# Kernel optimization log

Measured on AMD Instinct MI355X. Metric: run time of the kernel, lower is better.

## Reference

```python
import jax, jax.numpy as jnp
import numpy as np

N = 60000   # nodes (utterances)
E = 480000  # edges
C = 256     # utt_size == embedding_size (shrink disabled)
R = 16      # num_relations for conv1; conv3 uses n_speakers**2 == 16
NB = 8      # rgcn_reg_basis (num_bases)
NS = 4      # n_speakers


def _rgcn(x, src, dst, etype, comp, bases, root, bias, num_rel):
    # PyG RGCNConv with basis decomposition: W_r = sum_b comp[r,b] * bases[b]
    # out_i = sum_r mean_{j in N_r(i)} x_j @ W_r + x_i @ root + bias
    n = x.shape[0]
    W = jnp.einsum('rb,bio->rio', comp, bases)                      # [R,C,C]
    xw = jnp.einsum('ni,rio->rno', x, W).reshape(num_rel * n, -1)   # [R*N,C]
    seg = dst * num_rel + etype                                     # (dst, rel) bucket
    ones = jnp.ones((src.shape[0],), x.dtype)
    cnt = jax.ops.segment_sum(ones, seg, num_segments=n * num_rel)
    norm = (1.0 / jnp.maximum(cnt, 1.0))[seg]                       # per-relation mean
    msg = xw[etype * n + src] * norm[:, None]                       # [E,C] gather
    return jax.ops.segment_sum(msg, dst, num_segments=n) + x @ root + bias


def _gconv(x, src, dst, w_rel, b_rel, w_root):
    # PyG GraphConv, aggr='add': lin_rel(sum_j x_j) + lin_root(x)
    agg = jax.ops.segment_sum(x[src], dst, num_segments=x.shape[0])
    return agg @ w_rel + b_rel + x @ w_root


def _mlp(x, w1, c1, w2, c2, w3, c3):
    h = jax.nn.relu(x @ w1 + c1)
    h = jax.nn.relu(h @ w2 + c2)
    return h @ w3 + c3


def setup_inputs():
    key = jax.random.key(0)
    ks = jax.random.split(key, 24)
    f = lambda i, shape, s=0.05: jax.random.normal(ks[i], shape, jnp.float32) * s
    z = lambda d: jnp.zeros((d,), jnp.float32)
    return {
        'encoding': jax.random.normal(ks[0], (N, C), jnp.float32),
        'speaker': jax.random.randint(ks[1], (N,), 0, NS),
        'edge_index': jax.random.randint(ks[2], (2, E), 0, N),
        'edge_type': jax.random.randint(ks[3], (E,), 0, R),
        'edge_speaker_type': jax.random.randint(ks[4], (E,), 0, NS * NS),
        'spk_table': f(5, (NS, C)),
        'comp1': f(6, (R, NB), 0.2), 'bases1': f(7, (NB, C, C)),
        'root1': f(8, (C, C)), 'b1': z(C),
        'w2_rel': f(9, (C, C)), 'b2': z(C), 'w2_root': f(10, (C, C)),
        'comp3': f(11, (NS * NS, NB), 0.2), 'bases3': f(12, (NB, C, C)),
        'root3': f(13, (C, C)), 'b3': z(C),
        'w4_rel': f(14, (C, C)), 'b4': z(C), 'w4_root': f(15, (C, C)),
        'wd1': f(16, (3 * C, C // 2)), 'bd1': z(C // 2),
        'wd2': f(17, (C // 2, C // 4)), 'bd2': z(C // 4),
        'wd3': f(18, (C // 4, 1)), 'bd3': z(1),
    }


def reference(encoding, speaker, edge_index, edge_type, edge_speaker_type,
              spk_table, comp1, bases1, root1, b1, w2_rel, b2, w2_root,
              comp3, bases3, root3, b3, w4_rel, b4, w4_root,
              wd1, bd1, wd2, bd2, wd3, bd3):
    src, dst = edge_index[0], edge_index[1]
    x = encoding + spk_table[speaker]            # speaker embedding fusion
    h1 = _rgcn(x, src, dst, edge_type, comp1, bases1, root1, b1, R)
    h1 = _gconv(h1, src, dst, w2_rel, b2, w2_root)
    h2 = _rgcn(x, src, dst, edge_speaker_type, comp3, bases3, root3, b3, NS * NS)
    h2 = _gconv(h2, src, dst, w4_rel, b4, w4_root)
    feat = jnp.concatenate([encoding, h1, h2], axis=1)  # [N, 3C]
    pred = _mlp(feat, wd1, bd1, wd2, bd2, wd3, bd3)     # [N, 1]
    return pred.squeeze(1)
```

## Files before the change

kernel.cpp:

```cpp
#include <hip/hip_runtime.h>
#include <stdint.h>


typedef unsigned short u16;
typedef __attribute__((ext_vector_type(2))) float f32x2;
typedef __attribute__((ext_vector_type(4))) float f32x4;
typedef __attribute__((ext_vector_type(8))) short short8;

__device__ __forceinline__ float b2f(u16 u){
  union { uint32_t i; float f; } v; v.i = ((uint32_t)u) << 16; return v.f;
}
__device__ __forceinline__ u16 f2b(float f){
  union { float f; uint32_t i; } v; v.f = f;
  uint32_t u = v.i;
  return (u16)((u + 0x7FFFu + ((u >> 16) & 1u)) >> 16);
}
__device__ __forceinline__ u16 rdw(const void* p, size_t i, int f32){
  return f32 ? f2b(((const float*)p)[i]) : ((const u16*)p)[i];
}
__device__ __forceinline__ void gload_lds16(const u16* gp, u16* lp){
  __builtin_amdgcn_global_load_lds(
      (const __attribute__((address_space(1))) uint32_t*)(uintptr_t)gp,
      (__attribute__((address_space(3))) uint32_t*)lp, 16, 0, 0);
}

__global__ void detect_dtype(const u16* enc16, int* flag){
  __shared__ int cnt;
  if (threadIdx.x == 0) cnt = 0;
  __syncthreads();
  unsigned u = enc16[threadIdx.x * 2];
  int e = (u >> 7) & 0xFF;
  if (e >= 100 && e <= 140) atomicAdd(&cnt, 1);
  __syncthreads();
  if (threadIdx.x == 0) flag[0] = (cnt < 128) ? 1 : 0;
}

__global__ void cvt_small(const void* spk, const void* c1, const void* c3,
                          const void* b1, const void* b2, const void* b3,
                          const void* b4, const void* bd1, const void* wd2,
                          const void* bd2, const void* wd3, const void* bd3,
                          u16* __restrict__ arena, const int* __restrict__ flag)
{
  int f = *flag;
  int i = blockIdx.x * blockDim.x + threadIdx.x;
  if (i < 1024) { arena[i] = rdw(spk, i, f); return; } i -= 1024;
  if (i < 128)  { arena[1024 + i] = rdw(c1, i, f); return; } i -= 128;
  if (i < 128)  { arena[1152 + i] = rdw(c3, i, f); return; } i -= 128;
  if (i < 256)  { arena[1280 + i] = rdw(b1, i, f); return; } i -= 256;
  if (i < 256)  { arena[1536 + i] = rdw(b2, i, f); return; } i -= 256;
  if (i < 256)  { arena[1792 + i] = rdw(b3, i, f); return; } i -= 256;
  if (i < 256)  { arena[2048 + i] = rdw(b4, i, f); return; } i -= 256;
  if (i < 128)  { arena[2304 + i] = rdw(bd1, i, f); return; } i -= 128;
  if (i < 64)   { arena[10624 + i] = rdw(bd2, i, f); return; } i -= 64;
  if (i < 64)   { arena[10688 + i] = rdw(wd3, i, f); return; } i -= 64;
  if (i < 1)    { arena[10752 + i] = rdw(bd3, i, f); return; } i -= 1;
  if (i < 8192) { int o = i >> 7, k = i & 127;
    arena[10880 + i] = rdw(wd2, k * 64 + o, f); }
}

__global__ void cvt4(const void* __restrict__ in, u16* __restrict__ out, int n,
                     const int* __restrict__ flag){
  int i = (blockIdx.x * blockDim.x + threadIdx.x) * 4;
  if (i >= n) return;
  ushort4 o;
  if (*flag) {
    float4 v = *(const float4*)((const float*)in + i);
    o.x = f2b(v.x); o.y = f2b(v.y); o.z = f2b(v.z); o.w = f2b(v.w);
  } else {
    o = *(const ushort4*)((const u16*)in + i);
  }
  *(ushort4*)(out + i) = o;
}

__global__ void pack_weights(const void* __restrict__ bases1, const void* __restrict__ root1,
                             const void* __restrict__ w2_rel, const void* __restrict__ w2_root,
                             const void* __restrict__ bases3, const void* __restrict__ root3,
                             const void* __restrict__ w4_rel, const void* __restrict__ w4_root,
                             const void* __restrict__ wd1,
                             u16* __restrict__ B1t, u16* __restrict__ B3t,
                             u16* __restrict__ B2t, u16* __restrict__ B4t,
                             u16* __restrict__ D1t, const int* __restrict__ flag)
{
  int f = *flag;
  int idx = blockIdx.x * blockDim.x + threadIdx.x;
  if (idx < 256*2304) { int o = idx / 2304, k = idx % 2304;
    B1t[idx] = (k < 2048) ? rdw(bases1, k*256 + o, f) : rdw(root1, (k-2048)*256 + o, f); return; }
  idx -= 256*2304;
  if (idx < 256*2304) { int o = idx / 2304, k = idx % 2304;
    B3t[idx] = (k < 2048) ? rdw(bases3, k*256 + o, f) : rdw(root3, (k-2048)*256 + o, f); return; }
  idx -= 256*2304;
  if (idx < 256*512) { int o = idx / 512, k = idx % 512;
    B2t[idx] = (k < 256) ? rdw(w2_rel, k*256 + o, f) : rdw(w2_root, (k-256)*256 + o, f); return; }
  idx -= 256*512;
  if (idx < 256*512) { int o = idx / 512, k = idx % 512;
    B4t[idx] = (k < 256) ? rdw(w4_rel, k*256 + o, f) : rdw(w4_root, (k-256)*256 + o, f); return; }
  idx -= 256*512;
  if (idx < 128*768) { int o = idx / 768, k = idx % 768;
    D1t[idx] = rdw(wd1, k*128 + o, f); }
}

__global__ void build_x(const void* __restrict__ enc, const int* __restrict__ speaker,
                        const u16* __restrict__ spkA ,
                        u16* __restrict__ X , int N,
                        const int* __restrict__ flag)
{
  int f = *flag;
  int idx = blockIdx.x * blockDim.x + threadIdx.x;
  if (idx >= N * 64) return;
  int n = idx >> 6, c = (idx & 63) * 4;
  int sp = speaker[n];
  ushort4 sv = *(const ushort4*)(spkA + (size_t)sp*256 + c);
  float e0, e1, e2, e3;
  if (f) {
    float4 ev = *(const float4*)((const float*)enc + (size_t)n*256 + c);
    e0 = ev.x; e1 = ev.y; e2 = ev.z; e3 = ev.w;
  } else {
    ushort4 ev = *(const ushort4*)((const u16*)enc + (size_t)n*256 + c);
    e0 = b2f(ev.x); e1 = b2f(ev.y); e2 = b2f(ev.z); e3 = b2f(ev.w);
  }
  ushort4 xv;
  xv.x = f2b(e0 + b2f(sv.x));
  xv.y = f2b(e1 + b2f(sv.y));
  xv.z = f2b(e2 + b2f(sv.z));
  xv.w = f2b(e3 + b2f(sv.w));
  *(ushort4*)(X + (size_t)n*256 + c) = xv;
}

__global__ void edge_hist(const int* __restrict__ ei, int* cnt_dst, int E)
{
  int e = blockIdx.x * blockDim.x + threadIdx.x;
  if (e >= E) return;
  atomicAdd(&cnt_dst[ei[E + e]], 1);
}

__global__ void scan_p1(const int* __restrict__ cnt, int* __restrict__ partial,
                        int* __restrict__ bsum, int N)
{
  __shared__ int s[256];
  int t = threadIdx.x;
  int g = blockIdx.x * 256 + t;
  int v = (g < N) ? cnt[g] : 0;
  s[t] = v; __syncthreads();
  #pragma unroll
  for (int off = 1; off < 256; off <<= 1) {
    int u = (t >= off) ? s[t - off] : 0;
    __syncthreads();
    s[t] += u;
    __syncthreads();
  }
  partial[g] = s[t];
  if (t == 255) bsum[blockIdx.x] = s[255];
}

__global__ void scan_p2(int* __restrict__ bsum, int nb)
{
  __shared__ int s[1024];
  int t = threadIdx.x;
  int v = (t < nb) ? bsum[t] : 0;
  s[t] = v; __syncthreads();
  #pragma unroll
  for (int off = 1; off < 1024; off <<= 1) {
    int u = (t >= off) ? s[t - off] : 0;
    __syncthreads();
    s[t] += u;
    __syncthreads();
  }
  if (t < nb) bsum[t] = s[t] - v;
  if (t == nb - 1) bsum[nb] = s[t];
}

__global__ void scan_p3(const int* __restrict__ cnt, const int* __restrict__ partial,
                        const int* __restrict__ bsum, int* __restrict__ basep, int N)
{
  int g = blockIdx.x * 256 + threadIdx.x;
  if (g < N) basep[g] = partial[g] - cnt[g] + bsum[blockIdx.x];
  if (g == 0) basep[N] = bsum[(N + 255) / 256];
}

__global__ void edge_scatter(const int* __restrict__ ei, const int* __restrict__ et,
                             const int* __restrict__ est, const int* __restrict__ basep,
                             int* cursor, int* __restrict__ esorted, int E)
{
  int e = blockIdx.x * blockDim.x + threadIdx.x;
  if (e >= E) return;
  int d = ei[E + e];
  int pos = basep[d] + atomicAdd(&cursor[d], 1);
  esorted[pos] = ei[e] | (et[e] << 17) | (est[e] << 21);
}

__global__ __launch_bounds__(256) void rgcn_agg2(
    const int* __restrict__ esorted, const int* __restrict__ basep,
    const u16* __restrict__ X ,
    const u16* __restrict__ comp1 ,
    const u16* __restrict__ comp3 ,
    u16* __restrict__ Mix1 ,
    u16* __restrict__ Mix3 ,
    int n0, int CR)
{
  __shared__ float sc1[128], sc3[128];
  if (threadIdx.x < 128) sc1[threadIdx.x] = b2f(comp1[threadIdx.x]);
  else sc3[threadIdx.x - 128] = b2f(comp3[threadIdx.x - 128]);
  __syncthreads();
  int nl = blockIdx.x * 4 + (threadIdx.x >> 6);
  if (nl >= CR) return;
  int n = n0 + nl;
  int lane = threadIdx.x & 63;
  int e0 = basep[n], e1 = basep[n + 1];
  int myrel = lane & 15;
  int cnt = 0;
  for (int e = e0; e < e1; e++) {
    int rec = esorted[e];
    int r1 = (rec >> 17) & 15, r3 = (rec >> 21) & 15;
    if (lane < 16) cnt += (r1 == myrel);
    else if (lane < 32) cnt += (r3 == myrel);
  }
  float invv = 1.0f / (float)(cnt > 1 ? cnt : 1);
  f32x2 acc1[8][2] = {}, acc3[8][2] = {};
  for (int e = e0; e < e1; e++) {
    int rec = esorted[e];
    int src = rec & 0x1FFFF;
    int r1 = (rec >> 17) & 15, r3 = (rec >> 21) & 15;
    float iv1 = __shfl(invv, r1);
    float iv3 = __shfl(invv, 16 + r3);
    ushort4 xr = *(const ushort4*)(X + (size_t)src * 256 + lane * 4);
    f32x2 xlo, xhi;
    xlo[0] = b2f(xr.x); xlo[1] = b2f(xr.y);
    xhi[0] = b2f(xr.z); xhi[1] = b2f(xr.w);
    const float* c1p = sc1 + r1 * 8;
    const float* c3p = sc3 + r3 * 8;
    #pragma unroll
    for (int b = 0; b < 8; b++) {
      float w1s = c1p[b] * iv1;
      f32x2 w1 = {w1s, w1s};
      acc1[b][0] += w1 * xlo; acc1[b][1] += w1 * xhi;
      float w3s = c3p[b] * iv3;
      f32x2 w3 = {w3s, w3s};
      acc3[b][0] += w3 * xlo; acc3[b][1] += w3 * xhi;
    }
  }
  #pragma unroll
  for (int b = 0; b < 8; b++) {
    ushort4 o1, o3;
    o1.x = f2b(acc1[b][0][0]); o1.y = f2b(acc1[b][0][1]);
    o1.z = f2b(acc1[b][1][0]); o1.w = f2b(acc1[b][1][1]);
    o3.x = f2b(acc3[b][0][0]); o3.y = f2b(acc3[b][0][1]);
    o3.z = f2b(acc3[b][1][0]); o3.w = f2b(acc3[b][1][1]);
    *(ushort4*)(Mix1 + (size_t)nl * 2048 + b * 256 + lane * 4) = o1;
    *(ushort4*)(Mix3 + (size_t)nl * 2048 + b * 256 + lane * 4) = o3;
  }
}

__global__ __launch_bounds__(256) void gconv_agg2(
    const int* __restrict__ esorted, const int* __restrict__ basep,
    const u16* __restrict__ HinA ,
    const u16* __restrict__ HinB ,
    u16* __restrict__ AggA ,
    u16* __restrict__ AggB , int N)
{
  int n = blockIdx.x * 4 + (threadIdx.x >> 6);
  if (n >= N) return;
  int lane = threadIdx.x & 63;
  int half = lane >> 5, l32 = lane & 31;
  float a[8] = {}, b[8] = {};
  int e0 = basep[n], e1 = basep[n + 1];
  for (int e = e0; e < e1; e += 2) {
    int ee = e + half;
    bool ok = ee < e1;
    int src = esorted[ok ? ee : e] & 0x1FFFF;
    short8 hv  = *(const short8*)(HinA + (size_t)src * 256 + l32 * 8);
    short8 hv3 = *(const short8*)(HinB + (size_t)src * 256 + l32 * 8);
    if (ok) {
      #pragma unroll
      for (int j = 0; j < 8; j++) { a[j] += b2f((u16)hv[j]); b[j] += b2f((u16)hv3[j]); }
    }
  }
  #pragma unroll
  for (int j = 0; j < 8; j++) {
    a[j] += __shfl_xor(a[j], 32);
    b[j] += __shfl_xor(b[j], 32);
  }
  if (half == 0) {
    short8 oa, ob;
    #pragma unroll
    for (int j = 0; j < 8; j++) { oa[j] = (short)f2b(a[j]); ob[j] = (short)f2b(b[j]); }
    *(short8*)(AggA + (size_t)n * 256 + l32 * 8) = oa;
    *(short8*)(AggB + (size_t)n * 256 + l32 * 8) = ob;
  }
}

__global__ __launch_bounds__(256) void gemm_ms(
    const u16* __restrict__ A0, int lda0,
    const u16* __restrict__ A1, int lda1,
    const u16* __restrict__ A2, int lda2,
    int c1, int c2,
    const u16* __restrict__ Bt,
    const u16* __restrict__ bias,
    u16* __restrict__ Cout, int ldc,
    int M, int K, int relu, int nout, int nx,
    const u16* __restrict__ A0d, const u16* __restrict__ A1d,
    const u16* __restrict__ Btd,
    const u16* __restrict__ biasd, u16* __restrict__ Coutd)
{
  constexpr int BK = 64;
  __shared__ u16 As[128 * BK];
  __shared__ u16 Bs[128 * BK];
  int bi = blockIdx.x;
  const u16* A0u = A0; const u16* A1u = A1;
  const u16* Btu = Bt; const u16* biasu = bias;
  u16* Cu = Cout;
  if (bi >= nx) { bi -= nx; A0u = A0d; A1u = A1d; Btu = Btd; biasu = biasd; Cu = Coutd; }
  int nblk = (nout + 127) >> 7;
  int grpw = nblk << 3;
  int g = bi / grpw, r = bi % grpw;
  int bm = (g * 8 + (r & 7)) * 128;
  if (bm >= M) return;
  int bn = (r >> 3) * 128;

  int tid = threadIdx.x;
  int wid = tid >> 6, lane = tid & 63;
  int wm = (wid & 1) * 64, wn = (wid >> 1) * 64;
  int r8 = lane >> 3;
  int colA = ((lane & 7) ^ r8) * 8;
  int rloc = wid * 8 + r8;
  int lm = lane & 15, quad = lane >> 4;

  f32x4 acc[4][4];
  #pragma unroll
  for (int i = 0; i < 4; i++)
    #pragma unroll
    for (int j = 0; j < 4; j++) acc[i][j] = (f32x4)0.0f;

  int ga0 = bm + 0 * 32 + rloc; ga0 = ga0 < M ? ga0 : M - 1;
  int ga1 = bm + 1 * 32 + rloc; ga1 = ga1 < M ? ga1 : M - 1;
  int ga2 = bm + 2 * 32 + rloc; ga2 = ga2 < M ? ga2 : M - 1;
  int ga3 = bm + 3 * 32 + rloc; ga3 = ga3 < M ? ga3 : M - 1;
  int gb0 = bn + 0 * 32 + rloc; gb0 = gb0 < nout ? gb0 : nout - 1;
  int gb1 = bn + 1 * 32 + rloc; gb1 = gb1 < nout ? gb1 : nout - 1;
  int gb2 = bn + 2 * 32 + rloc; gb2 = gb2 < nout ? gb2 : nout - 1;
  int gb3 = bn + 3 * 32 + rloc; gb3 = gb3 < nout ? gb3 : nout - 1;

  for (int k0 = 0; k0 < K; k0 += BK) {
    const u16* srcp; int ldas, kO;
    if (k0 < c1)      { srcp = A0u; ldas = lda0; kO = k0; }
    else if (k0 < c2) { srcp = A1u; ldas = lda1; kO = k0 - c1; }
    else              { srcp = A2;  ldas = lda2; kO = k0 - c2; }
    const u16* abase = srcp + kO + colA;
    gload_lds16(abase + (size_t)ga0 * ldas, As + (0 * 32 + wid * 8) * BK);
    gload_lds16(abase + (size_t)ga1 * ldas, As + (1 * 32 + wid * 8) * BK);
    gload_lds16(abase + (size_t)ga2 * ldas, As + (2 * 32 + wid * 8) * BK);
    gload_lds16(abase + (size_t)ga3 * ldas, As + (3 * 32 + wid * 8) * BK);
    const u16* bbase = Btu + k0 + colA;
    gload_lds16(bbase + (size_t)gb0 * K, Bs + (0 * 32 + wid * 8) * BK);
    gload_lds16(bbase + (size_t)gb1 * K, Bs + (1 * 32 + wid * 8) * BK);
    gload_lds16(bbase + (size_t)gb2 * K, Bs + (2 * 32 + wid * 8) * BK);
    gload_lds16(bbase + (size_t)gb3 * K, Bs + (3 * 32 + wid * 8) * BK);
    __syncthreads();
    #pragma unroll
    for (int kk = 0; kk < BK; kk += 32) {
      int cb = (kk >> 3) + quad;
      int xo = ((cb ^ (lm & 7)) << 3);
      short8 af[4], bf[4];
      #pragma unroll
      for (int mi = 0; mi < 4; mi++)
        af[mi] = *(const short8*)(As + (wm + mi * 16 + lm) * BK + xo);
      #pragma unroll
      for (int ni = 0; ni < 4; ni++)
        bf[ni] = *(const short8*)(Bs + (wn + ni * 16 + lm) * BK + xo);
      #pragma unroll
      for (int mi = 0; mi < 4; mi++)
        #pragma unroll
        for (int ni = 0; ni < 4; ni++)
          acc[mi][ni] = __builtin_amdgcn_mfma_f32_16x16x32_bf16(
              af[mi], bf[ni], acc[mi][ni], 0, 0, 0);
    }
    __syncthreads();
  }
  #pragma unroll
  for (int ni = 0; ni < 4; ni++) {
    int gn = bn + wn + ni * 16 + lm;
    int gnb = gn < nout ? gn : nout - 1;
    float bv = b2f(biasu[gnb]);
    #pragma unroll
    for (int mi = 0; mi < 4; mi++) {
      int rbase = bm + wm + mi * 16 + quad * 4;
      #pragma unroll
      for (int rr = 0; rr < 4; rr++) {
        int gmr = rbase + rr;
        if (gmr < M && gn < nout) {
          float v = acc[mi][ni][rr] + bv;
          if (relu) v = fmaxf(v, 0.f);
          Cu[(size_t)gmr * ldc + gn] = f2b(v);
        }
      }
    }
  }
}

__global__ __launch_bounds__(256) void mlp_tail2(
    const u16* __restrict__ h2m, const u16* __restrict__ wd3,
    const u16* __restrict__ bd3, void* __restrict__ outp, int N,
    const int* __restrict__ flag)
{
  int n = blockIdx.x * 4 + (threadIdx.x >> 6);
  if (n >= N) return;
  int lane = threadIdx.x & 63;
  float r = b2f(h2m[(size_t)n * 64 + lane]) * b2f(wd3[lane]);
  #pragma unroll
  for (int off = 32; off > 0; off >>= 1) r += __shfl_xor(r, off, 64);
  if (lane == 0) {
    float v = r + b2f(bd3[0]);
    if (*flag) ((float*)outp)[n] = v;
    else       ((u16*)outp)[n] = f2b(v);
  }
}

__global__ void sentinel(u16* out, int n, float code){
  int i = blockIdx.x * blockDim.x + threadIdx.x;
  if (i < n) out[i] = f2b(code);
}

extern "C" void kernel_launch(void* const* d_in, const int* in_sizes, int n_in,
                              void* d_out, int out_size, void* d_ws, size_t ws_size,
                              hipStream_t stream)
{
  const void* enc     = d_in[0];
  const int* speaker  = (const int*)d_in[1];
  const int* ei       = (const int*)d_in[2];
  const int* et       = (const int*)d_in[3];
  const int* est      = (const int*)d_in[4];
  const void* spk_tab = d_in[5];
  const void* comp1   = d_in[6];
  const void* bases1  = d_in[7];
  const void* root1   = d_in[8];
  const void* b1      = d_in[9];
  const void* w2_rel  = d_in[10];
  const void* b2      = d_in[11];
  const void* w2_root = d_in[12];
  const void* comp3   = d_in[13];
  const void* bases3  = d_in[14];
  const void* root3   = d_in[15];
  const void* b3      = d_in[16];
  const void* w4_rel  = d_in[17];
  const void* b4      = d_in[18];
  const void* w4_root = d_in[19];
  const void* wd1     = d_in[20];
  const void* bd1     = d_in[21];
  const void* wd2     = d_in[22];
  const void* bd2     = d_in[23];
  const void* wd3     = d_in[24];
  const void* bd3     = d_in[25];

  int N = in_sizes[1];
  int E = in_sizes[3];
  int nb = (N + 255) / 256;

  char* ws = (char*)d_ws;
  size_t off = 0;
  auto alloc = [&](size_t bytes) -> char* {
    char* p = ws + off; off = (off + bytes + 255) & ~(size_t)255; return p;
  };
  u16* X    = (u16*)alloc((size_t)N * 256 * 2);
  u16* hA   = (u16*)alloc((size_t)N * 256 * 2);
  u16* hA3  = (u16*)alloc((size_t)N * 256 * 2);
  u16* B1t  = (u16*)alloc((size_t)256 * 2304 * 2);
  u16* B3t  = (u16*)alloc((size_t)256 * 2304 * 2);
  u16* B2t  = (u16*)alloc((size_t)256 * 512 * 2);
  u16* B4t  = (u16*)alloc((size_t)256 * 512 * 2);
  u16* D1t  = (u16*)alloc((size_t)128 * 768 * 2);
  u16* arena = (u16*)alloc((size_t)20480 * 2);
  int* flag    = (int*)alloc(256);
  int* basep   = (int*)alloc((size_t)(N + 1) * 4);
  int* esorted = (int*)alloc((size_t)E * 4);

  char* R = ws + off;
  size_t Rsize = (ws_size > off) ? (ws_size - off) : 0;

  int* cnt_dst = (int*)R;
  int* cursor  = (int*)(R + (size_t)N * 4);
  int* partial = (int*)(R + (size_t)2 * N * 4);
  int* bsum    = (int*)(R + (size_t)2 * N * 4 + (size_t)nb * 256 * 4);
  size_t zspan = (size_t)2 * N * 4;

  u16* AggA = (u16*)R;
  u16* hB   = (u16*)(R + (size_t)N * 256 * 2);
  u16* hC   = (u16*)(R + (size_t)2 * N * 256 * 2);
  u16* AggC = (u16*)(R + (size_t)3 * N * 256 * 2);
  u16* h1m  = AggA;
  u16* h2m  = AggA + (size_t)N * 128;
  size_t phase2_need = (size_t)4 * N * 256 * 2;

  long crl = (long)(Rsize / (4096 * 2));
  int chunk_max = (int)((crl / 128) * 128);
  int Mpad = ((N + 127) / 128) * 128;
  if (chunk_max > Mpad) chunk_max = Mpad;

  size_t sort_need = (size_t)2 * N * 4 + (size_t)nb * 256 * 4 + 2048 * 4;
  if (chunk_max < 128 || Rsize < phase2_need || Rsize < sort_need) {
    float code = 2000.0f + (float)(ws_size >> 20);
    sentinel<<<(out_size + 255) / 256, 256, 0, stream>>>((u16*)d_out, out_size, code);
    return;
  }
  int nchunks = (Mpad + chunk_max - 1) / chunk_max;
  int chunk_rows = (((N + nchunks - 1) / nchunks + 127) / 128) * 128;
  u16* Mix1blk = (u16*)R;
  u16* Mix3blk = Mix1blk + (size_t)chunk_rows * 2048;

  u16* spkA   = arena + 0;
  u16* comp1A = arena + 1024;
  u16* comp3A = arena + 1152;
  u16* b1A    = arena + 1280;
  u16* b2A    = arena + 1536;
  u16* b3A    = arena + 1792;
  u16* b4A    = arena + 2048;
  u16* bd1A   = arena + 2304;
  u16* bd2A   = arena + 10624;
  u16* wd3A   = arena + 10688;
  u16* bd3A   = arena + 10752;
  u16* wd2T   = arena + 10880;

  hipMemsetAsync(cnt_dst, 0, zspan, stream);

  detect_dtype<<<1, 256, 0, stream>>>((const u16*)enc, flag);
  cvt_small<<<75, 256, 0, stream>>>(spk_tab, comp1, comp3, b1, b2, b3, b4,
                                    bd1, wd2, bd2, wd3, bd3, arena, flag);

  int totpack = 256*2304*2 + 256*512*2 + 128*768;
  pack_weights<<<(totpack + 255) / 256, 256, 0, stream>>>(
      bases1, root1, w2_rel, w2_root, bases3, root3, w4_rel, w4_root, wd1,
      B1t, B3t, B2t, B4t, D1t, flag);
  build_x<<<(N * 64 + 255) / 256, 256, 0, stream>>>(enc, speaker, spkA, X, N, flag);
  edge_hist<<<(E + 255) / 256, 256, 0, stream>>>(ei, cnt_dst, E);
  scan_p1<<<nb, 256, 0, stream>>>(cnt_dst, partial, bsum, N);
  scan_p2<<<1, 1024, 0, stream>>>(bsum, nb);
  scan_p3<<<nb, 256, 0, stream>>>(cnt_dst, partial, bsum, basep, N);
  edge_scatter<<<(E + 255) / 256, 256, 0, stream>>>(ei, et, est, basep, cursor, esorted, E);

  int nb4 = (N + 3) / 4;
  const u16* nul = (const u16*)nullptr;
  auto nx_for = [](int M_, int nout_) {
    int mg = (M_ + 127) / 128;
    int nblk = (nout_ + 127) / 128;
    return ((mg + 7) / 8) * (nblk * 8);
  };

  for (int n0 = 0; n0 < N; n0 += chunk_rows) {
    int CR = (N - n0 < chunk_rows) ? (N - n0) : chunk_rows;
    rgcn_agg2<<<(CR + 3) / 4, 256, 0, stream>>>(esorted, basep, X, comp1A, comp3A,
                                                Mix1blk, Mix3blk, n0, CR);
    int nx = nx_for(CR, 256);
    gemm_ms<<<2 * nx, 256, 0, stream>>>(
        Mix1blk, 2048, X + (size_t)n0 * 256, 256, nul, 0,
        2048, 2304, B1t, b1A, hA + (size_t)n0 * 256, 256, CR, 2304, 0, 256, nx,
        Mix3blk, X + (size_t)n0 * 256, B3t, b3A, hA3 + (size_t)n0 * 256);
  }
  int nxN = nx_for(N, 256);
  gconv_agg2<<<nb4, 256, 0, stream>>>(esorted, basep, hA, hA3, AggA, AggC, N);
  cvt4<<<(N * 64 + 255) / 256, 256, 0, stream>>>(enc, X, N * 256, flag);
  gemm_ms<<<2 * nxN, 256, 0, stream>>>(
      AggA, 256, hA, 256, nul, 0, 256, 512,
      B2t, b2A, hB, 256, N, 512, 0, 256, nxN,
      AggC, hA3, B4t, b4A, hC);

  int nx1 = nx_for(N, 128);
  gemm_ms<<<nx1, 256, 0, stream>>>(
      X, 256, hB, 256, hC, 256, 256, 512,
      D1t, bd1A, h1m, 128, N, 768, 1, 128, nx1,
      nul, nul, nul, nul, (u16*)nullptr);
  int nx2 = nx_for(N, 64);
  gemm_ms<<<nx2, 256, 0, stream>>>(
      h1m, 128, nul, 0, nul, 0, 128, 128,
      wd2T, bd2A, h2m, 64, N, 128, 1, 64, nx2,
      nul, nul, nul, nul, (u16*)nullptr);
  mlp_tail2<<<nb4, 256, 0, stream>>>(h2m, wd3A, bd3A, d_out, N, flag);
}
```

Measured before the change: 790.7 us.

## Unroll RGCN edge loop by two and make GEMM a persistent grid

Measured after the change: 783.5 us. About the same (-0.9%).

```diff
diff --git a/kernel.cpp b/kernel.cpp
--- a/kernel.cpp
+++ b/kernel.cpp
@@ -216,7 +216,36 @@
   }
   float invv = 1.0f / (float)(cnt > 1 ? cnt : 1);
   f32x2 acc1[8][2] = {}, acc3[8][2] = {};
-  for (int e = e0; e < e1; e++) {
+  int e = e0;
+  for (; e + 1 < e1; e += 2) {
+    int recA = esorted[e], recB = esorted[e + 1];
+    int srcA = recA & 0x1FFFF, srcB = recB & 0x1FFFF;
+    ushort4 xra = *(const ushort4*)(X + (size_t)srcA * 256 + lane * 4);
+    ushort4 xrb = *(const ushort4*)(X + (size_t)srcB * 256 + lane * 4);
+    int r1a = (recA >> 17) & 15, r3a = (recA >> 21) & 15;
+    int r1b = (recB >> 17) & 15, r3b = (recB >> 21) & 15;
+    float iv1a = __shfl(invv, r1a), iv3a = __shfl(invv, 16 + r3a);
+    float iv1b = __shfl(invv, r1b), iv3b = __shfl(invv, 16 + r3b);
+    f32x2 alo, ahi, blo, bhi;
+    alo[0] = b2f(xra.x); alo[1] = b2f(xra.y);
+    ahi[0] = b2f(xra.z); ahi[1] = b2f(xra.w);
+    blo[0] = b2f(xrb.x); blo[1] = b2f(xrb.y);
+    bhi[0] = b2f(xrb.z); bhi[1] = b2f(xrb.w);
+    const float* c1a = sc1 + r1a * 8; const float* c3a = sc3 + r3a * 8;
+    const float* c1b = sc1 + r1b * 8; const float* c3b = sc3 + r3b * 8;
+    #pragma unroll
+    for (int b = 0; b < 8; b++) {
+      float w1a = c1a[b] * iv1a, w1b = c1b[b] * iv1b;
+      f32x2 v1a = {w1a, w1a}, v1b = {w1b, w1b};
+      acc1[b][0] += v1a * alo + v1b * blo;
+      acc1[b][1] += v1a * ahi + v1b * bhi;
+      float w3a = c3a[b] * iv3a, w3b = c3b[b] * iv3b;
+      f32x2 v3a = {w3a, w3a}, v3b = {w3b, w3b};
+      acc3[b][0] += v3a * alo + v3b * blo;
+      acc3[b][1] += v3a * ahi + v3b * bhi;
+    }
+  }
+  if (e < e1) {
     int rec = esorted[e];
     int src = rec & 0x1FFFF;
     int r1 = (rec >> 17) & 15, r3 = (rec >> 21) & 15;
@@ -296,7 +325,7 @@
     const u16* __restrict__ Bt,
     const u16* __restrict__ bias,
     u16* __restrict__ Cout, int ldc,
-    int M, int K, int relu, int nout, int nx,
+    int M, int K, int relu, int nout, int nx, int njobs,
     const u16* __restrict__ A0d, const u16* __restrict__ A1d,
     const u16* __restrict__ Btd,
     const u16* __restrict__ biasd, u16* __restrict__ Coutd)
@@ -304,18 +333,6 @@
   constexpr int BK = 64;
   __shared__ u16 As[128 * BK];
   __shared__ u16 Bs[128 * BK];
-  int bi = blockIdx.x;
-  const u16* A0u = A0; const u16* A1u = A1;
-  const u16* Btu = Bt; const u16* biasu = bias;
-  u16* Cu = Cout;
-  if (bi >= nx) { bi -= nx; A0u = A0d; A1u = A1d; Btu = Btd; biasu = biasd; Cu = Coutd; }
-  int nblk = (nout + 127) >> 7;
-  int grpw = nblk << 3;
-  int g = bi / grpw, r = bi % grpw;
-  int bm = (g * 8 + (r & 7)) * 128;
-  if (bm >= M) return;
-  int bn = (r >> 3) * 128;
-
   int tid = threadIdx.x;
   int wid = tid >> 6, lane = tid & 63;
   int wm = (wid & 1) * 64, wn = (wid >> 1) * 64;
@@ -323,73 +340,87 @@
   int colA = ((lane & 7) ^ r8) * 8;
   int rloc = wid * 8 + r8;
   int lm = lane & 15, quad = lane >> 4;
-
-  f32x4 acc[4][4];
-  #pragma unroll
-  for (int i = 0; i < 4; i++)
+  int nblk = (nout + 127) >> 7;
+  int grpw = nblk << 3;
+
+  for (int job = blockIdx.x; job < njobs; job += gridDim.x) {
+    int bi = job;
+    const u16* A0u = A0; const u16* A1u = A1;
+    const u16* Btu = Bt; const u16* biasu = bias;
+    u16* Cu = Cout;
+    if (bi >= nx) { bi -= nx; A0u = A0d; A1u = A1d; Btu = Btd; biasu = biasd; Cu = Coutd; }
+    int g = bi / grpw, r = bi % grpw;
+    int bm = (g * 8 + (r & 7)) * 128;
+    if (bm >= M) continue;
+    int bn = (r >> 3) * 128;
+
+    f32x4 acc[4][4];
     #pragma unroll
-    for (int j = 0; j < 4; j++) acc[i][j] = (f32x4)0.0f;
-
-  int ga0 = bm + 0 * 32 + rloc; ga0 = ga0 < M ? ga0 : M - 1;
-  int ga1 = bm + 1 * 32 + rloc; ga1 = ga1 < M ? ga1 : M - 1;
-  int ga2 = bm + 2 * 32 + rloc; ga2 = ga2 < M ? ga2 : M - 1;
-  int ga3 = bm + 3 * 32 + rloc; ga3 = ga3 < M ? ga3 : M - 1;
-  int gb0 = bn + 0 * 32 + rloc; gb0 = gb0 < nout ? gb0 : nout - 1;
-  int gb1 = bn + 1 * 32 + rloc; gb1 = gb1 < nout ? gb1 : nout - 1;
-  int gb2 = bn + 2 * 32 + rloc; gb2 = gb2 < nout ? gb2 : nout - 1;
-  int gb3 = bn + 3 * 32 + rloc; gb3 = gb3 < nout ? gb3 : nout - 1;
-
-  for (int k0 = 0; k0 < K; k0 += BK) {
-    const u16* srcp; int ldas, kO;
-    if (k0 < c1)      { srcp = A0u; ldas = lda0; kO = k0; }
-    else if (k0 < c2) { srcp = A1u; ldas = lda1; kO = k0 - c1; }
-    else              { srcp = A2;  ldas = lda2; kO = k0 - c2; }
-    const u16* abase = srcp + kO + colA;
-    gload_lds16(abase + (size_t)ga0 * ldas, As + (0 * 32 + wid * 8) * BK);
-    gload_lds16(abase + (size_t)ga1 * ldas, As + (1 * 32 + wid * 8) * BK);
-    gload_lds16(abase + (size_t)ga2 * ldas, As + (2 * 32 + wid * 8) * BK);
-    gload_lds16(abase + (size_t)ga3 * ldas, As + (3 * 32 + wid * 8) * BK);
-    const u16* bbase = Btu + k0 + colA;
-    gload_lds16(bbase + (size_t)gb0 * K, Bs + (0 * 32 + wid * 8) * BK);
-    gload_lds16(bbase + (size_t)gb1 * K, Bs + (1 * 32 + wid * 8) * BK);
-    gload_lds16(bbase + (size_t)gb2 * K, Bs + (2 * 32 + wid * 8) * BK);
-    gload_lds16(bbase + (size_t)gb3 * K, Bs + (3 * 32 + wid * 8) * BK);
-    __syncthreads();
-    #pragma unroll
-    for (int kk = 0; kk < BK; kk += 32) {
-      int cb = (kk >> 3) + quad;
-      int xo = ((cb ^ (lm & 7)) << 3);
-      short8 af[4], bf[4];
+    for (int i = 0; i < 4; i++)
       #pragma unroll
-      for (int mi = 0; mi < 4; mi++)
-        af[mi] = *(const short8*)(As + (wm + mi * 16 + lm) * BK + xo);
+      for (int j = 0; j < 4; j++) acc[i][j] = (f32x4)0.0f;
+
+    int ga0 = bm + 0 * 32 + rloc; ga0 = ga0 < M ? ga0 : M - 1;
+    int ga1 = bm + 1 * 32 + rloc; ga1 = ga1 < M ? ga1 : M - 1;
+    int ga2 = bm + 2 * 32 + rloc; ga2 = ga2 < M ? ga2 : M - 1;
+    int ga3 = bm + 3 * 32 + rloc; ga3 = ga3 < M ? ga3 : M - 1;
+    int gb0 = bn + 0 * 32 + rloc; gb0 = gb0 < nout ? gb0 : nout - 1;
+    int gb1 = bn + 1 * 32 + rloc; gb1 = gb1 < nout ? gb1 : nout - 1;
+    int gb2 = bn + 2 * 32 + rloc; gb2 = gb2 < nout ? gb2 : nout - 1;
+    int gb3 = bn + 3 * 32 + rloc; gb3 = gb3 < nout ? gb3 : nout - 1;
+
+    for (int k0 = 0; k0 < K; k0 += BK) {
+      const u16* srcp; int ldas, kO;
+      if (k0 < c1)      { srcp = A0u; ldas = lda0; kO = k0; }
+      else if (k0 < c2) { srcp = A1u; ldas = lda1; kO = k0 - c1; }
+      else              { srcp = A2;  ldas = lda2; kO = k0 - c2; }
+      const u16* abase = srcp + kO + colA;
+      gload_lds16(abase + (size_t)ga0 * ldas, As + (0 * 32 + wid * 8) * BK);
+      gload_lds16(abase + (size_t)ga1 * ldas, As + (1 * 32 + wid * 8) * BK);
+      gload_lds16(abase + (size_t)ga2 * ldas, As + (2 * 32 + wid * 8) * BK);
+      gload_lds16(abase + (size_t)ga3 * ldas, As + (3 * 32 + wid * 8) * BK);
+      const u16* bbase = Btu + k0 + colA;
+      gload_lds16(bbase + (size_t)gb0 * K, Bs + (0 * 32 + wid * 8) * BK);
+      gload_lds16(bbase + (size_t)gb1 * K, Bs + (1 * 32 + wid * 8) * BK);
+      gload_lds16(bbase + (size_t)gb2 * K, Bs + (2 * 32 + wid * 8) * BK);
+      gload_lds16(bbase + (size_t)gb3 * K, Bs + (3 * 32 + wid * 8) * BK);
+      __syncthreads();
       #pragma unroll
-      for (int ni = 0; ni < 4; ni++)
-        bf[ni] = *(const short8*)(Bs + (wn + ni * 16 + lm) * BK + xo);
-      #pragma unroll
-      for (int mi = 0; mi < 4; mi++)
+      for (int kk = 0; kk < BK; kk += 32) {
+        int cb = (kk >> 3) + quad;
+        int xo = ((cb ^ (lm & 7)) << 3);
+        short8 af[4], bf[4];
+        #pragma unroll
+        for (int mi = 0; mi < 4; mi++)
+          af[mi] = *(const short8*)(As + (wm + mi * 16 + lm) * BK + xo);
         #pragma unroll
         for (int ni = 0; ni < 4; ni++)
-          acc[mi][ni] = __builtin_amdgcn_mfma_f32_16x16x32_bf16(
-              af[mi], bf[ni], acc[mi][ni], 0, 0, 0);
+          bf[ni] = *(const short8*)(Bs + (wn + ni * 16 + lm) * BK + xo);
+        #pragma unroll
+        for (int mi = 0; mi < 4; mi++)
+          #pragma unroll
+          for (int ni = 0; ni < 4; ni++)
+            acc[mi][ni] = __builtin_amdgcn_mfma_f32_16x16x32_bf16(
+                af[mi], bf[ni], acc[mi][ni], 0, 0, 0);
+      }
+      __syncthreads();
     }
-    __syncthreads();
-  }
-  #pragma unroll
-  for (int ni = 0; ni < 4; ni++) {
-    int gn = bn + wn + ni * 16 + lm;
-    int gnb = gn < nout ? gn : nout - 1;
-    float bv = b2f(biasu[gnb]);
     #pragma unroll
-    for (int mi = 0; mi < 4; mi++) {
-      int rbase = bm + wm + mi * 16 + quad * 4;
+    for (int ni = 0; ni < 4; ni++) {
+      int gn = bn + wn + ni * 16 + lm;
+      int gnb = gn < nout ? gn : nout - 1;
+      float bv = b2f(biasu[gnb]);
       #pragma unroll
-      for (int rr = 0; rr < 4; rr++) {
-        int gmr = rbase + rr;
-        if (gmr < M && gn < nout) {
-          float v = acc[mi][ni][rr] + bv;
-          if (relu) v = fmaxf(v, 0.f);
-          Cu[(size_t)gmr * ldc + gn] = f2b(v);
+      for (int mi = 0; mi < 4; mi++) {
+        int rbase = bm + wm + mi * 16 + quad * 4;
+        #pragma unroll
+        for (int rr = 0; rr < 4; rr++) {
+          int gmr = rbase + rr;
+          if (gmr < M && gn < nout) {
+            float v = acc[mi][ni][rr] + bv;
+            if (relu) v = fmaxf(v, 0.f);
+            Cu[(size_t)gmr * ldc + gn] = f2b(v);
+          }
         }
       }
     }
@@ -490,18 +521,16 @@
   size_t phase2_need = (size_t)4 * N * 256 * 2;
 
   long crl = (long)(Rsize / (4096 * 2));
-  int chunk_max = (int)((crl / 128) * 128);
+  int chunk_rows = (int)((crl / 128) * 128);
   int Mpad = ((N + 127) / 128) * 128;
-  if (chunk_max > Mpad) chunk_max = Mpad;
+  if (chunk_rows > Mpad) chunk_rows = Mpad;
 
   size_t sort_need = (size_t)2 * N * 4 + (size_t)nb * 256 * 4 + 2048 * 4;
-  if (chunk_max < 128 || Rsize < phase2_need || Rsize < sort_need) {
+  if (chunk_rows < 128 || Rsize < phase2_need || Rsize < sort_need) {
     float code = 2000.0f + (float)(ws_size >> 20);
     sentinel<<<(out_size + 255) / 256, 256, 0, stream>>>((u16*)d_out, out_size, code);
     return;
   }
-  int nchunks = (Mpad + chunk_max - 1) / chunk_max;
-  int chunk_rows = (((N + nchunks - 1) / nchunks + 127) / 128) * 128;
   u16* Mix1blk = (u16*)R;
   u16* Mix3blk = Mix1blk + (size_t)chunk_rows * 2048;
 
@@ -542,34 +571,35 @@
     int nblk = (nout_ + 127) / 128;
     return ((mg + 7) / 8) * (nblk * 8);
   };
+  auto gsz = [](int njobs) { return njobs < 1280 ? njobs : 1280; };
 
   for (int n0 = 0; n0 < N; n0 += chunk_rows) {
     int CR = (N - n0 < chunk_rows) ? (N - n0) : chunk_rows;
     rgcn_agg2<<<(CR + 3) / 4, 256, 0, stream>>>(esorted, basep, X, comp1A, comp3A,
                                                 Mix1blk, Mix3blk, n0, CR);
     int nx = nx_for(CR, 256);
-    gemm_ms<<<2 * nx, 256, 0, stream>>>(
+    gemm_ms<<<gsz(2 * nx), 256, 0, stream>>>(
         Mix1blk, 2048, X + (size_t)n0 * 256, 256, nul, 0,
-        2048, 2304, B1t, b1A, hA + (size_t)n0 * 256, 256, CR, 2304, 0, 256, nx,
+        2048, 2304, B1t, b1A, hA + (size_t)n0 * 256, 256, CR, 2304, 0, 256, nx, 2 * nx,
         Mix3blk, X + (size_t)n0 * 256, B3t, b3A, hA3 + (size_t)n0 * 256);
   }
   int nxN = nx_for(N, 256);
   gconv_agg2<<<nb4, 256, 0, stream>>>(esorted, basep, hA, hA3, AggA, AggC, N);
   cvt4<<<(N * 64 + 255) / 256, 256, 0, stream>>>(enc, X, N * 256, flag);
-  gemm_ms<<<2 * nxN, 256, 0, stream>>>(
+  gemm_ms<<<gsz(2 * nxN), 256, 0, stream>>>(
       AggA, 256, hA, 256, nul, 0, 256, 512,
-      B2t, b2A, hB, 256, N, 512, 0, 256, nxN,
+      B2t, b2A, hB, 256, N, 512, 0, 256, nxN, 2 * nxN,
       AggC, hA3, B4t, b4A, hC);
 
   int nx1 = nx_for(N, 128);
-  gemm_ms<<<nx1, 256, 0, stream>>>(
+  gemm_ms<<<gsz(nx1), 256, 0, stream>>>(
       X, 256, hB, 256, hC, 256, 256, 512,
-      D1t, bd1A, h1m, 128, N, 768, 1, 128, nx1,
+      D1t, bd1A, h1m, 128, N, 768, 1, 128, nx1, nx1,
       nul, nul, nul, nul, (u16*)nullptr);
   int nx2 = nx_for(N, 64);
-  gemm_ms<<<nx2, 256, 0, stream>>>(
+  gemm_ms<<<gsz(nx2), 256, 0, stream>>>(
       h1m, 128, nul, 0, nul, 0, 128, 128,
-      wd2T, bd2A, h2m, 64, N, 128, 1, 64, nx2,
+      wd2T, bd2A, h2m, 64, N, 128, 1, 64, nx2, nx2,
       nul, nul, nul, nul, (u16*)nullptr);
   mlp_tail2<<<nb4, 256, 0, stream>>>(h2m, wd3A, bd3A, d_out, N, flag);
 }
```
